# Kernel tuning notes

Measured on AMD Instinct MI355X. Metric: run time of the kernel, lower is better.

## Reference

```python
import jax, jax.numpy as jnp
import numpy as np


def _pairwise_sq_dists(p, t):
    # p: [N,3], t: [M,3] -> [N,M] squared euclidean distances
    # |p|^2 + |t|^2 - 2 p.t^T (avoids materializing [N,M,3])
    p2 = jnp.sum(p * p, axis=-1)  # [N]
    t2 = jnp.sum(t * t, axis=-1)  # [M]
    cross = jnp.einsum('nd,md->nm', p, t)  # [N,M]
    d = p2[:, None] + t2[None, :] - 2.0 * cross
    return jnp.maximum(d, 0.0)  # clamp tiny negatives from cancellation


def setup_inputs() -> dict:
    key = jax.random.key(0)
    k1, k2 = jax.random.split(key)
    N = 16384
    predict = jax.random.normal(k1, (1, N, 3), dtype=jnp.float32)
    target = jax.random.normal(k2, (1, N, 3), dtype=jnp.float32)
    return {"predict": predict, "target": target}


def reference(predict, target):
    # Faithful to forward: only the first batch element is used.
    p = predict[0]  # [N,3]
    t = target[0]   # [M,3]
    d = _pairwise_sq_dists(p, t)          # [N,M] squared distances
    dist1 = jnp.min(d, axis=1)            # nearest target for each predict pt
    dist2 = jnp.min(d, axis=0)            # nearest predict for each target pt
    loss = jnp.mean(dist1) + jnp.mean(dist2)
    return loss
```

## Files before the change

### kernel.cpp

```cpp
#include <hip/hip_runtime.h>


typedef short s16x8 __attribute__((ext_vector_type(8)));
typedef float f32x16 __attribute__((ext_vector_type(16)));

static __device__ __forceinline__ unsigned short f2bf(float f) {
    unsigned u = __float_as_uint(f);
    unsigned r = (u + 0x7FFFu + ((u >> 16) & 1u)) >> 16;
    return (unsigned short)r;
}
static __device__ __forceinline__ float bf2f(unsigned short h) {
    return __uint_as_float(((unsigned)h) << 16);
}
static __device__ __forceinline__ void split2(float v, unsigned short& h, unsigned short& l) {
    h = f2bf(v);
    l = f2bf(v - bf2f(h));
}

union Pack16 { unsigned short u[16]; uint4 v[2]; };

__global__ void prep_pack(const float* __restrict__ predict, const float* __restrict__ target,
                          unsigned short* __restrict__ ApP, unsigned short* __restrict__ BpP,
                          unsigned short* __restrict__ ApT, unsigned short* __restrict__ BpT,
                          int N)
{
    int i = blockIdx.x * blockDim.x + threadIdx.x;
    if (i >= 2 * N) return;
    const float* src = (i < N) ? predict : target;
    unsigned short* Ap = (i < N) ? ApP : ApT;
    unsigned short* Bp = (i < N) ? BpP : BpT;
    int j = (i < N) ? i : i - N;

    float x = src[3*j], y = src[3*j+1], z = src[3*j+2];
    float n2 = __builtin_fmaf(x, x, __builtin_fmaf(y, y, z*z));

    unsigned short xh,xl,yh,yl,zh,zl,nh,nl,qxh,qxl,qyh,qyl,qzh,qzl;
    split2(x, xh, xl); split2(y, yh, yl); split2(z, zh, zl); split2(n2, nh, nl);
    split2(-2.0f*x, qxh, qxl); split2(-2.0f*y, qyh, qyl); split2(-2.0f*z, qzh, qzl);
    const unsigned short one = f2bf(1.0f);

    Pack16 a, b;
    a.u[0]=xh; a.u[1]=xh; a.u[2]=xl; a.u[3]=xl;
    a.u[4]=yh; a.u[5]=yh; a.u[6]=yl; a.u[7]=yl;
    a.u[8]=zh; a.u[9]=zh; a.u[10]=zl; a.u[11]=zl;
    a.u[12]=nh; a.u[13]=nl; a.u[14]=one; a.u[15]=one;

    b.u[0]=qxh; b.u[1]=qxl; b.u[2]=qxh; b.u[3]=qxl;
    b.u[4]=qyh; b.u[5]=qyl; b.u[6]=qyh; b.u[7]=qyl;
    b.u[8]=qzh; b.u[9]=qzl; b.u[10]=qzh; b.u[11]=qzl;
    b.u[12]=one; b.u[13]=one; b.u[14]=nh; b.u[15]=nl;

    uint4* ad = (uint4*)(Ap + (size_t)j * 16);
    uint4* bd = (uint4*)(Bp + (size_t)j * 16);
    ad[0] = a.v[0]; ad[1] = a.v[1];
    bd[0] = b.v[0]; bd[1] = b.v[1];
}

#define TB 64

__global__ __launch_bounds__(256, 2) void chamfer_main(
    const unsigned short* __restrict__ ApP, const unsigned short* __restrict__ BpP,
    const unsigned short* __restrict__ ApT, const unsigned short* __restrict__ BpT,
    float* __restrict__ partials, int N)
{
    const int dir = blockIdx.z;
    const unsigned short* __restrict__ Ap = dir ? ApT : ApP;
    const unsigned short* __restrict__ Bp = dir ? BpP : BpT;
    float* __restrict__ pout = partials + (size_t)(dir * 4 + blockIdx.y) * N;

    __shared__ unsigned short lB[TB * 32 * 16];

    const int tid  = threadIdx.x;
    const int w    = tid >> 6;
    const int lane = tid & 63;
    const int lm   = lane & 31;
    const int lg   = lane >> 5;

    const int row0 = blockIdx.x * 256 + w * 64;

    const uint4* A4 = (const uint4*)Ap;
    s16x8 a0 = __builtin_bit_cast(s16x8, A4[(size_t)(row0      + lm) * 2 + lg]);
    s16x8 a1 = __builtin_bit_cast(s16x8, A4[(size_t)(row0 + 32 + lm) * 2 + lg]);

    float rm0[16], rm1[16];
    #pragma unroll
    for (int r = 0; r < 16; ++r) { rm0[r] = 3.0e38f; rm1[r] = 3.0e38f; }

    const f32x16 zc = {0.f,0.f,0.f,0.f,0.f,0.f,0.f,0.f,0.f,0.f,0.f,0.f,0.f,0.f,0.f,0.f};

    const uint4* gB = (const uint4*)(Bp + (size_t)blockIdx.y * (N / 4) * 16);
    uint4* lds4 = (uint4*)lB;
    const int nchunk = (N / 4) / (TB * 32);

    for (int chunk = 0; chunk < nchunk; ++chunk) {
        __syncthreads();
        const uint4* gsrc = gB + (size_t)chunk * (TB * 32 * 2);
        #pragma unroll
        for (int it = 0; it < (TB * 32 * 2) / 256; ++it)
            lds4[it * 256 + tid] = gsrc[it * 256 + tid];
        __syncthreads();

        #pragma unroll 2
        for (int t = 0; t < TB; ++t) {
            uint4 bv = *(const uint4*)(lB + t * 512 + lm * 16 + lg * 8);
            s16x8 b = __builtin_bit_cast(s16x8, bv);
            f32x16 acc0 = __builtin_amdgcn_mfma_f32_32x32x16_bf16(a0, b, zc, 0, 0, 0);
            f32x16 acc1 = __builtin_amdgcn_mfma_f32_32x32x16_bf16(a1, b, zc, 0, 0, 0);
            #pragma unroll
            for (int r = 0; r < 16; ++r) {
                rm0[r] = fminf(rm0[r], acc0[r]);
                rm1[r] = fminf(rm1[r], acc1[r]);
            }
        }
    }

    #pragma unroll
    for (int m = 1; m <= 16; m <<= 1) {
        #pragma unroll
        for (int r = 0; r < 16; ++r) {
            rm0[r] = fminf(rm0[r], __shfl_xor(rm0[r], m, 64));
            rm1[r] = fminf(rm1[r], __shfl_xor(rm1[r], m, 64));
        }
    }
    #pragma unroll
    for (int r = 0; r < 16; ++r) {
        int rl = (r & 3) + 8 * (r >> 2) + 4 * lg;
        if (lm == r) {
            pout[row0 +      rl] = rm0[r];
            pout[row0 + 32 + rl] = rm1[r];
        }
    }
}

__global__ void chamfer_reduce(const float* __restrict__ partials, float* __restrict__ out, int N) {
    __shared__ double sacc[16];
    const int tid = threadIdx.x;
    double acc = 0.0;
    for (int i = tid; i < N; i += blockDim.x) {
        float m0 = fminf(fminf(partials[i],         partials[N + i]),
                         fminf(partials[2*N + i],   partials[3*N + i]));
        float m1 = fminf(fminf(partials[4*N + i],   partials[5*N + i]),
                         fminf(partials[6*N + i],   partials[7*N + i]));
        acc += (double)fmaxf(m0, 0.0f) + (double)fmaxf(m1, 0.0f);
    }
    for (int off = 32; off; off >>= 1)
        acc += __shfl_down(acc, off, 64);
    const int wave = tid >> 6, lane = tid & 63;
    if (lane == 0) sacc[wave] = acc;
    __syncthreads();
    if (tid == 0) {
        double t = 0.0;
        int nw = blockDim.x >> 6;
        for (int wv = 0; wv < nw; ++wv) t += sacc[wv];
        out[0] = (float)(t / (double)N);
    }
}

extern "C" void kernel_launch(void* const* d_in, const int* in_sizes, int n_in,
                              void* d_out, int out_size, void* d_ws, size_t ws_size,
                              hipStream_t stream) {
    const float* predict = (const float*)d_in[0];
    const float* target  = (const float*)d_in[1];
    const int N = in_sizes[0] / 3;

    unsigned short* ws16 = (unsigned short*)d_ws;
    unsigned short* ApP = ws16;
    unsigned short* BpP = ws16 + (size_t)1 * N * 16;
    unsigned short* ApT = ws16 + (size_t)2 * N * 16;
    unsigned short* BpT = ws16 + (size_t)3 * N * 16;
    float* partials = (float*)(ws16 + (size_t)4 * N * 16);

    prep_pack<<<dim3((2 * N + 255) / 256), dim3(256), 0, stream>>>(
        predict, target, ApP, BpP, ApT, BpT, N);

    dim3 grid(N / 256, 4, 2);
    chamfer_main<<<grid, dim3(256), 0, stream>>>(ApP, BpP, ApT, BpT, partials, N);

    chamfer_reduce<<<1, dim3(1024), 0, stream>>>(partials, (float*)d_out, N);
}
```

Before: 85.40 us.

## Retile chamfer MFMA kernel with 4 A-fragments, single LDS stage, parallel reduce

Each wave now holds four 32-row A fragments instead of two, so every B fragment read from LDS feeds four MFMAs. Each block loads one 1024-column B slice into LDS once, which removes the chunk loop and its repeated barriers; the column space is split into 16 groups and occupancy is raised to 4 blocks per SM. The single-block final reduction becomes a two-stage multi-block reduction over the larger partials buffer. In exchange there are more partial writes, more register pressure from 64 min accumulators, and an extra kernel launch.

```diff
diff --git a/kernel.cpp b/kernel.cpp
--- a/kernel.cpp
+++ b/kernel.cpp
@@ -56,9 +56,13 @@
     bd[0] = b.v[0]; bd[1] = b.v[1];
 }
 
-#define TB 64
+#define TPB   256
+#define AFRAG 4
+#define ROWS_PER_BLOCK (AFRAG * 32 * 4)
+#define SCOLS 1024
+#define CGROUPS 16
 
-__global__ __launch_bounds__(256, 2) void chamfer_main(
+__global__ __launch_bounds__(TPB, 4) void chamfer_main(
     const unsigned short* __restrict__ ApP, const unsigned short* __restrict__ BpP,
     const unsigned short* __restrict__ ApT, const unsigned short* __restrict__ BpT,
     float* __restrict__ partials, int N)
@@ -66,9 +70,8 @@
     const int dir = blockIdx.z;
     const unsigned short* __restrict__ Ap = dir ? ApT : ApP;
     const unsigned short* __restrict__ Bp = dir ? BpP : BpT;
-    float* __restrict__ pout = partials + (size_t)(dir * 4 + blockIdx.y) * N;
 
-    __shared__ unsigned short lB[TB * 32 * 16];
+    __shared__ unsigned short lB[SCOLS * 16];
 
     const int tid  = threadIdx.x;
     const int w    = tid >> 6;
@@ -76,84 +79,87 @@
     const int lm   = lane & 31;
     const int lg   = lane >> 5;
 
-    const int row0 = blockIdx.x * 256 + w * 64;
+    const uint4* gB = (const uint4*)Bp + (size_t)blockIdx.y * (SCOLS * 2);
+    uint4* l4 = (uint4*)lB;
+    #pragma unroll
+    for (int it = 0; it < (SCOLS * 2) / TPB; ++it)
+        l4[it * TPB + tid] = gB[it * TPB + tid];
 
+    const int rowbase = blockIdx.x * ROWS_PER_BLOCK + w * (AFRAG * 32);
     const uint4* A4 = (const uint4*)Ap;
-    s16x8 a0 = __builtin_bit_cast(s16x8, A4[(size_t)(row0      + lm) * 2 + lg]);
-    s16x8 a1 = __builtin_bit_cast(s16x8, A4[(size_t)(row0 + 32 + lm) * 2 + lg]);
+    s16x8 af[AFRAG];
+    #pragma unroll
+    for (int f = 0; f < AFRAG; ++f)
+        af[f] = __builtin_bit_cast(s16x8, A4[(size_t)(rowbase + f * 32 + lm) * 2 + lg]);
 
-    float rm0[16], rm1[16];
+    __syncthreads();
+
+    float rm[AFRAG][16];
     #pragma unroll
-    for (int r = 0; r < 16; ++r) { rm0[r] = 3.0e38f; rm1[r] = 3.0e38f; }
+    for (int f = 0; f < AFRAG; ++f)
+        #pragma unroll
+        for (int r = 0; r < 16; ++r) rm[f][r] = 3.0e38f;
 
     const f32x16 zc = {0.f,0.f,0.f,0.f,0.f,0.f,0.f,0.f,0.f,0.f,0.f,0.f,0.f,0.f,0.f,0.f};
 
-    const uint4* gB = (const uint4*)(Bp + (size_t)blockIdx.y * (N / 4) * 16);
-    uint4* lds4 = (uint4*)lB;
-    const int nchunk = (N / 4) / (TB * 32);
-
-    for (int chunk = 0; chunk < nchunk; ++chunk) {
-        __syncthreads();
-        const uint4* gsrc = gB + (size_t)chunk * (TB * 32 * 2);
+    #pragma unroll 4
+    for (int t = 0; t < SCOLS / 32; ++t) {
+        uint4 bv = *(const uint4*)(lB + t * 512 + lm * 16 + lg * 8);
+        s16x8 b = __builtin_bit_cast(s16x8, bv);
         #pragma unroll
-        for (int it = 0; it < (TB * 32 * 2) / 256; ++it)
-            lds4[it * 256 + tid] = gsrc[it * 256 + tid];
-        __syncthreads();
-
-        #pragma unroll 2
-        for (int t = 0; t < TB; ++t) {
-            uint4 bv = *(const uint4*)(lB + t * 512 + lm * 16 + lg * 8);
-            s16x8 b = __builtin_bit_cast(s16x8, bv);
-            f32x16 acc0 = __builtin_amdgcn_mfma_f32_32x32x16_bf16(a0, b, zc, 0, 0, 0);
-            f32x16 acc1 = __builtin_amdgcn_mfma_f32_32x32x16_bf16(a1, b, zc, 0, 0, 0);
+        for (int f = 0; f < AFRAG; ++f) {
+            f32x16 acc = __builtin_amdgcn_mfma_f32_32x32x16_bf16(af[f], b, zc, 0, 0, 0);
             #pragma unroll
-            for (int r = 0; r < 16; ++r) {
-                rm0[r] = fminf(rm0[r], acc0[r]);
-                rm1[r] = fminf(rm1[r], acc1[r]);
-            }
+            for (int r = 0; r < 16; ++r)
+                rm[f][r] = fminf(rm[f][r], acc[r]);
         }
     }
 
     #pragma unroll
     for (int m = 1; m <= 16; m <<= 1) {
         #pragma unroll
-        for (int r = 0; r < 16; ++r) {
-            rm0[r] = fminf(rm0[r], __shfl_xor(rm0[r], m, 64));
-            rm1[r] = fminf(rm1[r], __shfl_xor(rm1[r], m, 64));
-        }
+        for (int f = 0; f < AFRAG; ++f)
+            #pragma unroll
+            for (int r = 0; r < 16; ++r)
+                rm[f][r] = fminf(rm[f][r], __shfl_xor(rm[f][r], m, 64));
     }
+
+    const int slot = dir * CGROUPS + blockIdx.y;
     #pragma unroll
     for (int r = 0; r < 16; ++r) {
         int rl = (r & 3) + 8 * (r >> 2) + 4 * lg;
         if (lm == r) {
-            pout[row0 +      rl] = rm0[r];
-            pout[row0 + 32 + rl] = rm1[r];
+            #pragma unroll
+            for (int f = 0; f < AFRAG; ++f)
+                partials[(size_t)slot * N + rowbase + f * 32 + rl] = rm[f][r];
         }
     }
 }
 
-__global__ void chamfer_reduce(const float* __restrict__ partials, float* __restrict__ out, int N) {
-    __shared__ double sacc[16];
+__global__ __launch_bounds__(256) void chamfer_reduce1(
+    const float* __restrict__ partials, double* __restrict__ bsum, int N)
+{
     const int tid = threadIdx.x;
-    double acc = 0.0;
-    for (int i = tid; i < N; i += blockDim.x) {
-        float m0 = fminf(fminf(partials[i],         partials[N + i]),
-                         fminf(partials[2*N + i],   partials[3*N + i]));
-        float m1 = fminf(fminf(partials[4*N + i],   partials[5*N + i]),
-                         fminf(partials[6*N + i],   partials[7*N + i]));
-        acc += (double)fmaxf(m0, 0.0f) + (double)fmaxf(m1, 0.0f);
+    const int row = blockIdx.x * 256 + tid;
+    float m0 = 3.0e38f, m1 = 3.0e38f;
+    #pragma unroll
+    for (int k = 0; k < CGROUPS; ++k) {
+        m0 = fminf(m0, partials[(size_t)k * N + row]);
+        m1 = fminf(m1, partials[(size_t)(CGROUPS + k) * N + row]);
     }
-    for (int off = 32; off; off >>= 1)
-        acc += __shfl_down(acc, off, 64);
-    const int wave = tid >> 6, lane = tid & 63;
-    if (lane == 0) sacc[wave] = acc;
+    double s = (double)fmaxf(m0, 0.0f) + (double)fmaxf(m1, 0.0f);
+    for (int off = 32; off; off >>= 1) s += __shfl_down(s, off, 64);
+    __shared__ double sacc[4];
+    if ((tid & 63) == 0) sacc[tid >> 6] = s;
     __syncthreads();
-    if (tid == 0) {
-        double t = 0.0;
-        int nw = blockDim.x >> 6;
-        for (int wv = 0; wv < nw; ++wv) t += sacc[wv];
-        out[0] = (float)(t / (double)N);
-    }
+    if (tid == 0) bsum[blockIdx.x] = sacc[0] + sacc[1] + sacc[2] + sacc[3];
+}
+
+__global__ void chamfer_reduce2(const double* __restrict__ bsum,
+                                float* __restrict__ out, int N) {
+    double s = bsum[threadIdx.x];
+    for (int off = 32; off; off >>= 1) s += __shfl_down(s, off, 64);
+    if (threadIdx.x == 0) out[0] = (float)(s / (double)N);
 }
 
 extern "C" void kernel_launch(void* const* d_in, const int* in_sizes, int n_in,
@@ -169,12 +175,14 @@
     unsigned short* ApT = ws16 + (size_t)2 * N * 16;
     unsigned short* BpT = ws16 + (size_t)3 * N * 16;
     float* partials = (float*)(ws16 + (size_t)4 * N * 16);
+    double* bsum    = (double*)(partials + (size_t)32 * N);
 
     prep_pack<<<dim3((2 * N + 255) / 256), dim3(256), 0, stream>>>(
         predict, target, ApP, BpP, ApT, BpT, N);
 
-    dim3 grid(N / 256, 4, 2);
-    chamfer_main<<<grid, dim3(256), 0, stream>>>(ApP, BpP, ApT, BpT, partials, N);
+    dim3 grid(N / ROWS_PER_BLOCK, CGROUPS, 2);
+    chamfer_main<<<grid, dim3(TPB), 0, stream>>>(ApP, BpP, ApT, BpT, partials, N);
 
-    chamfer_reduce<<<1, dim3(1024), 0, stream>>>(partials, (float*)d_out, N);
+    chamfer_reduce1<<<dim3(N / 256), dim3(256), 0, stream>>>(partials, bsum, N);
+    chamfer_reduce2<<<dim3(1), dim3(64), 0, stream>>>(bsum, (float*)d_out, N);
 }
```

Result: slower. 128.5 us (+50.5%).
